# Kernel tuning notes

Measured on AMD Instinct MI355X. Metric: run time of the kernel, lower is better.

## Reference

```python
import jax, jax.numpy as jnp
import numpy as np

N_NODES = 100000
N_EDGE_PAIRS = 800000  # undirected pairs -> 1.6M directed edges
DIM_IN = 128
NUM_CLASSES = 16
N_ITERS = 5


def _log_normalize(a):
    return a - jax.nn.logsumexp(a, axis=-1, keepdims=True)


def setup_inputs() -> dict:
    key = jax.random.key(0)
    k1, k2, k3, k4, k5 = jax.random.split(key, 5)
    # reciprocal directed edges: edges 2i and 2i+1 are reverses of each other
    src = jax.random.randint(k1, (N_EDGE_PAIRS,), 0, N_NODES)
    dst = jax.random.randint(k2, (N_EDGE_PAIRS,), 0, N_NODES)
    e_src = jnp.stack([src, dst], axis=1).reshape(-1)  # [E]
    e_dst = jnp.stack([dst, src], axis=1).reshape(-1)  # [E]
    edge_index = jnp.stack([e_src, e_dst], axis=0)     # [2, E]
    E = e_src.shape[0]
    rv = jnp.arange(E).reshape(-1, 2)[:, ::-1].reshape(-1)  # reverse-edge permutation
    x = jax.random.normal(k3, (N_NODES, DIM_IN), dtype=jnp.float32)
    W = jax.random.normal(k4, (DIM_IN, NUM_CLASSES), dtype=jnp.float32) * 0.1
    b = jnp.zeros((NUM_CLASSES,), dtype=jnp.float32)
    dim_param = NUM_CLASSES * (NUM_CLASSES + 1) // 2
    param = jax.random.normal(k5, (dim_param,), dtype=jnp.float32) * 0.1
    return {"x": x, "W": W, "b": b, "param": param,
            "edge_index": edge_index, "rv": rv}


def reference(x, W, b, param, edge_index, rv):
    N = x.shape[0]
    C = W.shape[1]
    # MLP (num_hidden=0 -> single Linear) + LogSoftmax
    log_b0 = jax.nn.log_softmax(x @ W + b, axis=-1)  # [N, C]
    # coupling matrix logH (symmetric), detached since learn_coupling=False
    rid, cid = np.tril_indices(C)
    logT = jnp.zeros((C, C), dtype=x.dtype).at[rid, cid].set(
        jax.nn.log_sigmoid(param * 10.0))
    logH = logT + jnp.triu(logT.T, 1)
    logH = jax.lax.stop_gradient(logH)
    src, dst = edge_index[0], edge_index[1]
    E = src.shape[0]
    log_msg = jnp.full((E, C), -float(np.log(C)), dtype=x.dtype)
    log_b = log_b0
    for _ in range(N_ITERS):
        # message: gather beliefs at source, subtract reverse message
        t = log_b[src] - log_msg[rv]                                    # [E, C]
        raw = jax.nn.logsumexp(t[:, :, None] + logH[None, :, :], axis=1)  # [E, C]
        log_msg = _log_normalize(raw)
        # aggregate (scatter-add) into destination nodes, then update
        agg = jax.ops.segment_sum(log_msg, dst, num_segments=N)         # [N, C]
        log_b = _log_normalize(agg + log_b0)
    return log_b
```

## Files before the change

### kernel.cpp

```cpp
#include <hip/hip_runtime.h>
#include <hip/hip_fp16.h>
#include <math.h>

#define NN      100000
#define EE      1600000
#define DIN     128
#define CC      16
#define NITERS  5
#define NBLKS   100000
#define UU      5
#define GRID_E  (NBLKS / (UU * 4))
#define NEGLOGC (-2.772588722239781f)
#define QS      128.0f
#define QINV    (1.0f / 128.0f)
#define QCLAMP  8.0f
#define GRID_U  782

#define ROWF    32
#define ROWH    64
#define AGGH    32
#define ROWU    16
#define AGGU    8

#if __has_builtin(__builtin_amdgcn_mfma_f32_16x16x16bf16_1k)
#define USE_1K 1
#else
#define USE_1K 0
#endif

typedef float f4  __attribute__((ext_vector_type(4)));
typedef float v4f __attribute__((ext_vector_type(4)));
typedef short v4s __attribute__((ext_vector_type(4)));
typedef unsigned short u8h __attribute__((ext_vector_type(8)));
typedef unsigned long long ull;

__device__ __forceinline__ unsigned short f2h(float f) {
    return __half_as_ushort(__float2half(f));
}
__device__ __forceinline__ float h2f(unsigned short u) {
    return __half2float(__ushort_as_half(u));
}
__device__ __forceinline__ unsigned int pack_h(float lo, float hi) {
    return (unsigned int)f2h(lo) | ((unsigned int)f2h(hi) << 16);
}
__device__ __forceinline__ unsigned short f2bf(float f) {
    unsigned int u = __float_as_uint(f);
    unsigned int r = u + 0x7fffu + ((u >> 16) & 1u);
    return (unsigned short)(r >> 16);
}

__global__ __launch_bounds__(256) void k_setup(
    const float* __restrict__ x, const float* __restrict__ W,
    const float* __restrict__ b, const float* __restrict__ param,
    float* __restrict__ M, float* __restrict__ logb0,
    float* __restrict__ st)
{
    __shared__ float WT[CC][132];

    {
        f4 w0 = *(const f4*)(W + threadIdx.x * 8);
        f4 w1 = *(const f4*)(W + threadIdx.x * 8 + 4);
#pragma unroll
        for (int i = 0; i < 4; ++i) {
            int idx = threadIdx.x * 8 + i;
            WT[idx & 15][idx >> 4] = w0[i];
        }
#pragma unroll
        for (int i = 0; i < 4; ++i) {
            int idx = threadIdx.x * 8 + 4 + i;
            WT[idx & 15][idx >> 4] = w1[i];
        }
    }

    if (blockIdx.x == 0 && threadIdx.x < CC * (CC + 1) / 2) {
        int i = threadIdx.x;
        int r = 0;
        while ((r + 1) * (r + 2) / 2 <= i) ++r;
        int c = i - r * (r + 1) / 2;
        float z = param[i] * 10.0f;
        float s = 1.0f / (1.0f + __expf(-z));
        M[r * CC + c] = s;
        if (r != c) M[c * CC + r] = s;
    }

    __syncthreads();

    if (blockIdx.x == 0 && threadIdx.x < CC) {
        float s = 0.f;
        for (int c = 0; c < CC; ++c) s += M[threadIdx.x * CC + c];
        M[256 + threadIdx.x] = s;
    }

    int idx = blockIdx.x * 256 + threadIdx.x;
    int node = idx >> 4;
    int cls  = idx & 15;

    ((unsigned short*)st)[(long)node * ROWH + AGGH + cls] = 0;

    const f4* xr4 = (const f4*)(x + (long)node * DIN);
    const f4* wr4 = (const f4*)(&WT[cls][0]);
    float acc = b[cls];
#pragma unroll 8
    for (int k4 = 0; k4 < DIN / 4; ++k4) {
        f4 xv = __builtin_nontemporal_load(xr4 + k4);
        f4 wv = wr4[k4];
        acc = fmaf(xv.x, wv.x, acc);
        acc = fmaf(xv.y, wv.y, acc);
        acc = fmaf(xv.z, wv.z, acc);
        acc = fmaf(xv.w, wv.w, acc);
    }
    float m = acc;
    for (int off = 8; off; off >>= 1) m = fmaxf(m, __shfl_xor(m, off, 16));
    float s = __expf(acc - m);
    for (int off = 8; off; off >>= 1) s += __shfl_xor(s, off, 16);
    float lb = acc - m - __logf(s);
    logb0[idx] = lb;
    st[(long)node * ROWF + cls] = lb;
}

template <bool RD_MSG, bool WR_MSG>
__global__ __launch_bounds__(256) void k_edges_s(
    const int* __restrict__ esrc, const float* __restrict__ st,
    const float* __restrict__ Mg, ull* __restrict__ msg8)
{
    const int lane = threadIdx.x & 63;
    const int wid  = blockIdx.x * 4 + (threadIdx.x >> 6);
    const int m    = lane & 15;
    const int q    = lane >> 4;

    ull* stw = (ull*)st;

    const int ed = lane >> 2;
    const int j4 = lane & 3;
    const int sl = (j4 << 4) | ed;

#if USE_1K
    v4s mfrag;
#pragma unroll
    for (int jj = 0; jj < 4; ++jj)
        mfrag[jj] = (short)f2bf(Mg[m * CC + 4 * q + jj]);
#endif
    f4 rs = *(const f4*)(Mg + 256 + 4 * q);

    int srcv[UU];
    ull mw[UU];
#pragma unroll
    for (int u = 0; u < UU; ++u) {
        const long blk = (long)wid * UU + u;
        srcv[u] = __builtin_nontemporal_load(esrc + blk * 16 + m);
        if (RD_MSG)
            mw[u] = __builtin_nontemporal_load(msg8 + blk * 64 + q * 16 + (m ^ 1));
    }
    f4 lb[UU];
#pragma unroll
    for (int u = 0; u < UU; ++u)
        lb[u] = *(const f4*)(st + (long)srcv[u] * ROWF + 4 * q);

#pragma unroll
    for (int u = 0; u < UU; ++u) {
        const long blk = (long)wid * UU + u;

        float mv0 = 0.f, mv1 = 0.f, mv2 = 0.f, mv3 = 0.f;
        if (RD_MSG) {
            mv0 = h2f((unsigned short)(mw[u] & 0xffffu));
            mv1 = h2f((unsigned short)((mw[u] >> 16) & 0xffffu));
            mv2 = h2f((unsigned short)((mw[u] >> 32) & 0xffffu));
            mv3 = h2f((unsigned short)(mw[u] >> 48));
        }

        float e0 = __expf(lb[u].x - mv0);
        float e1f = __expf(lb[u].y - mv1);
        float e2 = __expf(lb[u].z - mv2);
        float e3 = __expf(lb[u].w - mv3);

        float Tm = e0 * rs.x;
        Tm = fmaf(e1f, rs.y, Tm);
        Tm = fmaf(e2, rs.z, Tm);
        Tm = fmaf(e3, rs.w, Tm);
        Tm += __shfl_xor(Tm, 16, 64);
        Tm += __shfl_xor(Tm, 32, 64);
        float lT = __logf(Tm);

        float D0, D1, D2, D3;
#if USE_1K
        v4s a;
        a[0] = (short)f2bf(e0); a[1] = (short)f2bf(e1f);
        a[2] = (short)f2bf(e2); a[3] = (short)f2bf(e3);
        v4f acc = {0.f, 0.f, 0.f, 0.f};
        v4f D = __builtin_amdgcn_mfma_f32_16x16x16bf16_1k(mfrag, a, acc, 0, 0, 0);
        D0 = D[0]; D1 = D[1]; D2 = D[2]; D3 = D[3];
#else
        float ee[4] = {e0, e1f, e2, e3};
        float g1[4], g2[4], g3[4];
#pragma unroll
        for (int jj = 0; jj < 4; ++jj) {
            g1[jj] = __shfl_xor(ee[jj], 16, 64);
            g2[jj] = __shfl_xor(ee[jj], 32, 64);
            g3[jj] = __shfl_xor(ee[jj], 48, 64);
        }
        float Dv[4];
#pragma unroll
        for (int i = 0; i < 4; ++i) {
            const float* Mr = Mg + (4 * q + i) * CC;
            float d = 0.f;
#pragma unroll
            for (int jj = 0; jj < 4; ++jj) {
                d = fmaf(Mr[4 * q + jj],       ee[jj], d);
                d = fmaf(Mr[4 * (q ^ 1) + jj], g1[jj], d);
                d = fmaf(Mr[4 * (q ^ 2) + jj], g2[jj], d);
                d = fmaf(Mr[4 * (q ^ 3) + jj], g3[jj], d);
            }
            Dv[i] = d;
        }
        D0 = Dv[0]; D1 = Dv[1]; D2 = Dv[2]; D3 = Dv[3];
#endif
        float n0 = __logf(D0) - lT;
        float n1 = __logf(D1) - lT;
        float n2 = __logf(D2) - lT;
        float n3 = __logf(D3) - lT;

        if (WR_MSG) {
            ull w = (ull)pack_h(n0, n1) | ((ull)pack_h(n2, n3) << 32);
            __builtin_nontemporal_store(w, msg8 + blk * 64 + q * 16 + m);
        }

        int dstv = __shfl_xor(srcv[u], 1, 16);

        unsigned int q0 = (unsigned int)(fminf(fmaxf(-n0, 0.f), QCLAMP) * QS + 0.5f);
        unsigned int q1 = (unsigned int)(fminf(fmaxf(-n1, 0.f), QCLAMP) * QS + 0.5f);
        unsigned int q2 = (unsigned int)(fminf(fmaxf(-n2, 0.f), QCLAMP) * QS + 0.5f);
        unsigned int q3 = (unsigned int)(fminf(fmaxf(-n3, 0.f), QCLAMP) * QS + 0.5f);
        ull p = (ull)q0 | ((ull)q1 << 16) | ((ull)q2 << 32) | ((ull)q3 << 48);

        ull v = __shfl(p, sl, 64);
        int d = __shfl(dstv, ed, 16);
        atomicAdd(&stw[(long)d * ROWU + AGGU + j4], v);
    }
}

template <bool FINAL>
__global__ __launch_bounds__(256) void k_update(
    const float* __restrict__ logb0, float* __restrict__ st,
    float* __restrict__ out)
{
    const int t = blockIdx.x * 256 + threadIdx.x;
    if (t >= 2 * NN) return;
    const int node = t >> 1;
    const int h    = t & 1;

    unsigned short* agg16 = (unsigned short*)st;
    const long ab = (long)node * ROWH + AGGH + h * 8;
    u8h av = *(const u8h*)(agg16 + ab);
    *(u8h*)(agg16 + ab) = (u8h){0,0,0,0,0,0,0,0};

    const long db = (long)node * CC + h * 8;
    f4 l0 = *(const f4*)(logb0 + db);
    f4 l1 = *(const f4*)(logb0 + db + 4);

    float v[8];
#pragma unroll
    for (int i = 0; i < 4; ++i) {
        v[i]     = fmaf(-(float)av[i],     QINV, l0[i]);
        v[4 + i] = fmaf(-(float)av[4 + i], QINV, l1[i]);
    }
    float mx = v[0];
#pragma unroll
    for (int i = 1; i < 8; ++i) mx = fmaxf(mx, v[i]);
    mx = fmaxf(mx, __shfl_xor(mx, 1, 64));

    float s = 0.f;
#pragma unroll
    for (int i = 0; i < 8; ++i) s += __expf(v[i] - mx);
    s += __shfl_xor(s, 1, 64);
    float lz = mx + __logf(s);

    f4 o0, o1;
#pragma unroll
    for (int i = 0; i < 4; ++i) { o0[i] = v[i] - lz; o1[i] = v[4 + i] - lz; }
    if (FINAL) {
        *(f4*)(out + db)     = o0;
        *(f4*)(out + db + 4) = o1;
    } else {
        float* bp = st + (long)node * ROWF + h * 8;
        *(f4*)(bp)     = o0;
        *(f4*)(bp + 4) = o1;
    }
}

extern "C" void kernel_launch(void* const* d_in, const int* in_sizes, int n_in,
                              void* d_out, int out_size, void* d_ws, size_t ws_size,
                              hipStream_t stream)
{
    const float* x     = (const float*)d_in[0];
    const float* W     = (const float*)d_in[1];
    const float* b     = (const float*)d_in[2];
    const float* param = (const float*)d_in[3];
    const int*   eidx  = (const int*)d_in[4];
    const int*   esrc  = eidx;

    char* ws = (char*)d_ws;
    float* M     = (float*)ws;
    float* st    = (float*)(ws + 4096);
    float* logb0 = (float*)(ws + 4096 + 12800000);
    ull*   msg8  = (ull*)(ws + 4096 + 12800000 + 6400000);
    float* outp  = (float*)d_out;

    k_setup<<<NN * CC / 256, 256, 0, stream>>>(x, W, b, param, M, logb0, st);

    for (int it = 0; it < NITERS; ++it) {
        if (it == 0)
            k_edges_s<false, true><<<GRID_E, 256, 0, stream>>>(
                esrc, st, M, msg8);
        else if (it == NITERS - 1)
            k_edges_s<true, false><<<GRID_E, 256, 0, stream>>>(
                esrc, st, M, msg8);
        else
            k_edges_s<true, true><<<GRID_E, 256, 0, stream>>>(
                esrc, st, M, msg8);
        if (it == NITERS - 1)
            k_update<true><<<GRID_U, 256, 0, stream>>>(logb0, st, outp);
        else
            k_update<false><<<GRID_U, 256, 0, stream>>>(logb0, st, outp);
    }
}
```

Measured before the change: 613.3 us.

## Fuse node update into edge kernel via quantized seeded triple-buffered accumulators

```diff
diff --git a/kernel.cpp b/kernel.cpp
--- a/kernel.cpp
+++ b/kernel.cpp
@@ -16,12 +16,6 @@
 #define QCLAMP  8.0f
 #define GRID_U  782
 
-#define ROWF    32
-#define ROWH    64
-#define AGGH    32
-#define ROWU    16
-#define AGGU    8
-
 #if __has_builtin(__builtin_amdgcn_mfma_f32_16x16x16bf16_1k)
 #define USE_1K 1
 #else
@@ -31,7 +25,6 @@
 typedef float f4  __attribute__((ext_vector_type(4)));
 typedef float v4f __attribute__((ext_vector_type(4)));
 typedef short v4s __attribute__((ext_vector_type(4)));
-typedef unsigned short u8h __attribute__((ext_vector_type(8)));
 typedef unsigned long long ull;
 
 __device__ __forceinline__ unsigned short f2h(float f) {
@@ -53,7 +46,8 @@
     const float* __restrict__ x, const float* __restrict__ W,
     const float* __restrict__ b, const float* __restrict__ param,
     float* __restrict__ M, float* __restrict__ logb0,
-    float* __restrict__ st)
+    unsigned short* __restrict__ seedq,
+    unsigned short* __restrict__ bufA, unsigned short* __restrict__ bufB)
 {
     __shared__ float WT[CC][132];
 
@@ -94,8 +88,6 @@
     int idx = blockIdx.x * 256 + threadIdx.x;
     int node = idx >> 4;
     int cls  = idx & 15;
-
-    ((unsigned short*)st)[(long)node * ROWH + AGGH + cls] = 0;
 
     const f4* xr4 = (const f4*)(x + (long)node * DIN);
     const f4* wr4 = (const f4*)(&WT[cls][0]);
@@ -114,21 +106,32 @@
     float s = __expf(acc - m);
     for (int off = 8; off; off >>= 1) s += __shfl_xor(s, off, 16);
     float lb = acc - m - __logf(s);
+
     logb0[idx] = lb;
-    st[(long)node * ROWF + cls] = lb;
-}
-
-template <bool RD_MSG, bool WR_MSG>
-__global__ __launch_bounds__(256) void k_edges_s(
-    const int* __restrict__ esrc, const float* __restrict__ st,
-    const float* __restrict__ Mg, ull* __restrict__ msg8)
+    unsigned short su = (unsigned short)(-lb * QS + 0.5f);
+    seedq[idx] = su;
+    bufA[idx]  = su;
+    bufB[idx]  = su;
+}
+
+template <bool RD_MSG, bool WR_MSG, bool RESEED>
+__global__ __launch_bounds__(256) void k_edges_f(
+    const int* __restrict__ esrc, const ull* __restrict__ Aprev,
+    ull* __restrict__ Acur, ull* __restrict__ Anext,
+    const ull* __restrict__ seedq, const float* __restrict__ Mg,
+    ull* __restrict__ msg8)
 {
     const int lane = threadIdx.x & 63;
     const int wid  = blockIdx.x * 4 + (threadIdx.x >> 6);
     const int m    = lane & 15;
     const int q    = lane >> 4;
 
-    ull* stw = (ull*)st;
+    if (RESEED) {
+        int gid = blockIdx.x * 256 + threadIdx.x;
+        if (gid < NN * 4)
+            __builtin_nontemporal_store(
+                __builtin_nontemporal_load(seedq + gid), Anext + gid);
+    }
 
     const int ed = lane >> 2;
     const int j4 = lane & 3;
@@ -151,14 +154,23 @@
         if (RD_MSG)
             mw[u] = __builtin_nontemporal_load(msg8 + blk * 64 + q * 16 + (m ^ 1));
     }
-    f4 lb[UU];
+    ull au[UU];
 #pragma unroll
     for (int u = 0; u < UU; ++u)
-        lb[u] = *(const f4*)(st + (long)srcv[u] * ROWF + 4 * q);
+        au[u] = Aprev[(long)srcv[u] * 4 + q];
 
 #pragma unroll
     for (int u = 0; u < UU; ++u) {
         const long blk = (long)wid * UU + u;
+
+        float v0 = -(float)(unsigned int)(au[u] & 0xffffu)         * QINV;
+        float v1 = -(float)(unsigned int)((au[u] >> 16) & 0xffffu) * QINV;
+        float v2 = -(float)(unsigned int)((au[u] >> 32) & 0xffffu) * QINV;
+        float v3 = -(float)(unsigned int)(au[u] >> 48)             * QINV;
+
+        float mx = fmaxf(fmaxf(v0, v1), fmaxf(v2, v3));
+        mx = fmaxf(mx, __shfl_xor(mx, 16, 64));
+        mx = fmaxf(mx, __shfl_xor(mx, 32, 64));
 
         float mv0 = 0.f, mv1 = 0.f, mv2 = 0.f, mv3 = 0.f;
         if (RD_MSG) {
@@ -168,10 +180,10 @@
             mv3 = h2f((unsigned short)(mw[u] >> 48));
         }
 
-        float e0 = __expf(lb[u].x - mv0);
-        float e1f = __expf(lb[u].y - mv1);
-        float e2 = __expf(lb[u].z - mv2);
-        float e3 = __expf(lb[u].w - mv3);
+        float e0  = __expf(v0 - mx - mv0);
+        float e1f = __expf(v1 - mx - mv1);
+        float e2  = __expf(v2 - mx - mv2);
+        float e3  = __expf(v3 - mx - mv3);
 
         float Tm = e0 * rs.x;
         Tm = fmaf(e1f, rs.y, Tm);
@@ -234,24 +246,22 @@
 
         ull v = __shfl(p, sl, 64);
         int d = __shfl(dstv, ed, 16);
-        atomicAdd(&stw[(long)d * ROWU + AGGU + j4], v);
-    }
-}
-
-template <bool FINAL>
-__global__ __launch_bounds__(256) void k_update(
-    const float* __restrict__ logb0, float* __restrict__ st,
-    float* __restrict__ out)
+        atomicAdd(&Acur[(long)d * 4 + j4], v);
+    }
+}
+
+__global__ __launch_bounds__(256) void k_final(
+    const float* __restrict__ logb0, const ull* __restrict__ Acur,
+    const ull* __restrict__ seedq, float* __restrict__ out)
 {
     const int t = blockIdx.x * 256 + threadIdx.x;
     if (t >= 2 * NN) return;
     const int node = t >> 1;
     const int h    = t & 1;
 
-    unsigned short* agg16 = (unsigned short*)st;
-    const long ab = (long)node * ROWH + AGGH + h * 8;
-    u8h av = *(const u8h*)(agg16 + ab);
-    *(u8h*)(agg16 + ab) = (u8h){0,0,0,0,0,0,0,0};
+    const long ab = (long)node * 4 + h * 2;
+    ull a0 = Acur[ab],  a1 = Acur[ab + 1];
+    ull s0 = seedq[ab], s1 = seedq[ab + 1];
 
     const long db = (long)node * CC + h * 8;
     f4 l0 = *(const f4*)(logb0 + db);
@@ -260,8 +270,10 @@
     float v[8];
 #pragma unroll
     for (int i = 0; i < 4; ++i) {
-        v[i]     = fmaf(-(float)av[i],     QINV, l0[i]);
-        v[4 + i] = fmaf(-(float)av[4 + i], QINV, l1[i]);
+        int d0 = (int)((a0 >> (16 * i)) & 0xffffu) - (int)((s0 >> (16 * i)) & 0xffffu);
+        int d1 = (int)((a1 >> (16 * i)) & 0xffffu) - (int)((s1 >> (16 * i)) & 0xffffu);
+        v[i]     = fmaf(-(float)d0, QINV, l0[i]);
+        v[4 + i] = fmaf(-(float)d1, QINV, l1[i]);
     }
     float mx = v[0];
 #pragma unroll
@@ -277,14 +289,8 @@
     f4 o0, o1;
 #pragma unroll
     for (int i = 0; i < 4; ++i) { o0[i] = v[i] - lz; o1[i] = v[4 + i] - lz; }
-    if (FINAL) {
-        *(f4*)(out + db)     = o0;
-        *(f4*)(out + db + 4) = o1;
-    } else {
-        float* bp = st + (long)node * ROWF + h * 8;
-        *(f4*)(bp)     = o0;
-        *(f4*)(bp + 4) = o1;
-    }
+    *(f4*)(out + db)     = o0;
+    *(f4*)(out + db + 4) = o1;
 }
 
 extern "C" void kernel_launch(void* const* d_in, const int* in_sizes, int n_in,
@@ -299,27 +305,31 @@
     const int*   esrc  = eidx;
 
     char* ws = (char*)d_ws;
-    float* M     = (float*)ws;
-    float* st    = (float*)(ws + 4096);
-    float* logb0 = (float*)(ws + 4096 + 12800000);
-    ull*   msg8  = (ull*)(ws + 4096 + 12800000 + 6400000);
-    float* outp  = (float*)d_out;
-
-    k_setup<<<NN * CC / 256, 256, 0, stream>>>(x, W, b, param, M, logb0, st);
-
-    for (int it = 0; it < NITERS; ++it) {
-        if (it == 0)
-            k_edges_s<false, true><<<GRID_E, 256, 0, stream>>>(
-                esrc, st, M, msg8);
-        else if (it == NITERS - 1)
-            k_edges_s<true, false><<<GRID_E, 256, 0, stream>>>(
-                esrc, st, M, msg8);
-        else
-            k_edges_s<true, true><<<GRID_E, 256, 0, stream>>>(
-                esrc, st, M, msg8);
-        if (it == NITERS - 1)
-            k_update<true><<<GRID_U, 256, 0, stream>>>(logb0, st, outp);
-        else
-            k_update<false><<<GRID_U, 256, 0, stream>>>(logb0, st, outp);
-    }
-}
+    float* M      = (float*)ws;
+    float* logb0  = (float*)(ws + 4096);
+    ull*   seedq  = (ull*)(ws + 6404096);
+    ull*   bufA   = (ull*)(ws + 9604096);
+    ull*   bufB   = (ull*)(ws + 12804096);
+    ull*   bufC   = (ull*)(ws + 16004096);
+    ull*   msg8   = (ull*)(ws + 19204096);
+    float* outp   = (float*)d_out;
+
+    ull* bufs[3] = { bufA, bufB, bufC };
+
+    k_setup<<<NN * CC / 256, 256, 0, stream>>>(
+        x, W, b, param, M, logb0, (unsigned short*)seedq,
+        (unsigned short*)bufA, (unsigned short*)bufB);
+
+    k_edges_f<false, true, true><<<GRID_E, 256, 0, stream>>>(
+        esrc, bufs[0], bufs[1], bufs[2], seedq, M, msg8);
+    k_edges_f<true, true, true><<<GRID_E, 256, 0, stream>>>(
+        esrc, bufs[1], bufs[2], bufs[0], seedq, M, msg8);
+    k_edges_f<true, true, true><<<GRID_E, 256, 0, stream>>>(
+        esrc, bufs[2], bufs[0], bufs[1], seedq, M, msg8);
+    k_edges_f<true, true, true><<<GRID_E, 256, 0, stream>>>(
+        esrc, bufs[0], bufs[1], bufs[2], seedq, M, msg8);
+    k_edges_f<true, false, false><<<GRID_E, 256, 0, stream>>>(
+        esrc, bufs[1], bufs[2], bufs[0], seedq, M, msg8);
+
+    k_final<<<GRID_U, 256, 0, stream>>>(logb0, bufs[2], seedq, outp);
+}
```

Result: faster. 521.8 us (-14.9%).
